# Kernel optimization log

Hardware: AMD Instinct MI355X
Metric: run time of the kernel (lower is better)

## Reference

```python
import jax, jax.numpy as jnp
import numpy as np

HIDDEN = 128
LR = 0.01          # epsilon (energy optimizer Adam lr)
B1, B2, EPS = 0.9, 0.999, 1e-8  # torch.optim.Adam defaults


def rho(s):
    return jnp.clip(s, 0.0, 1.0)


def setup_inputs() -> dict:
    key = jax.random.key(0)
    k_x, k_w0, k_w1 = jax.random.split(key, 3)
    input_size, output_size = 262144, 1024
    x = jax.random.uniform(k_x, (input_size,), dtype=jnp.float32)
    # xavier_uniform as in nn.init.xavier_uniform_
    lim0 = float(np.sqrt(6.0 / (input_size + HIDDEN)))
    W0 = jax.random.uniform(k_w0, (input_size, HIDDEN), jnp.float32, -lim0, lim0)
    lim1 = float(np.sqrt(6.0 / (HIDDEN + output_size)))
    W1 = jax.random.uniform(k_w1, (HIDDEN, output_size), jnp.float32, -lim1, lim1)
    b0 = jnp.zeros((input_size,), jnp.float32)
    b1 = jnp.zeros((HIDDEN,), jnp.float32)
    b2 = jnp.zeros((output_size,), jnp.float32)
    return {"x": x, "b0": b0, "b1": b1, "b2": b2, "W0": W0, "W1": W1,
            "n_iterations": 20}


def reference(x, b0, b1, b2, W0, W1, n_iterations):
    # Energy: sum ||rho(layer)||^2/2 - sum rho(layer).b - sum rho(pre) W rho(post)
    def energy(h, o):
        rx, rh, ro = rho(x), rho(h), rho(o)
        sq = 0.5 * (rx @ rx + rh @ rh + ro @ ro)
        lin = -(rx @ b0 + rh @ b1 + ro @ b2)
        quad = -((rx @ W0) @ rh + (rh @ W1) @ ro)
        return sq + lin + quad

    grad_e = jax.grad(energy, argnums=(0, 1))

    def adam_update(s, m, v, g, t):
        m = B1 * m + (1.0 - B1) * g
        v = B2 * v + (1.0 - B2) * (g * g)
        m_hat = m / (1.0 - jnp.power(jnp.float32(B1), t))
        v_hat = v / (1.0 - jnp.power(jnp.float32(B2), t))
        s = s - LR * m_hat / (jnp.sqrt(v_hat) + EPS)
        return s, m, v

    def step(carry, _):
        h, o, mh, vh, mo, vo, t = carry
        t = t + 1.0
        gh, go = grad_e(h, o)
        h, mh, vh = adam_update(h, mh, vh, gh, t)
        o, mo, vo = adam_update(o, mo, vo, go, t)
        return (h, o, mh, vh, mo, vo, t), None

    z_h = jnp.zeros_like(b1)  # hidden state starts at zeros
    z_o = jnp.zeros_like(b2)  # output state starts at zeros
    carry0 = (z_h, z_o, z_h, z_h, z_o, z_o, jnp.float32(0.0))
    (h, o, *_), _ = jax.lax.scan(step, carry0, None, length=int(n_iterations))
    return o
```

## Files before the change

kernel.cpp:

```cpp
#include <hip/hip_runtime.h>
#include <math.h>

#define NBLK_B 8

__device__ __forceinline__ float rho(float s) {
  return fminf(fmaxf(s, 0.0f), 1.0f);
}

__device__ __forceinline__ float drho(float s) {
  if (s < 0.0f || s > 1.0f) return 0.0f;
  float g = 1.0f;
  if (s == 0.0f) g *= 0.5f;
  if (s == 1.0f) g *= 0.5f;
  return g;
}

template <int ROWS>
__global__ __launch_bounds__(256) void k1_xw0(const float* __restrict__ x,
                                              const float* __restrict__ W0,
                                              float* __restrict__ part,
                                              int* __restrict__ flags) {
  __shared__ float xs[ROWS];
  __shared__ float red[8][132];
  const int t = threadIdx.x;
  const int b = blockIdx.x;
  if (b == 0 && t < NBLK_B) flags[t * 32] = 0;
  const int r0 = b * ROWS;
  for (int i = t; i < ROWS; i += 256) xs[i] = rho(x[r0 + i]);
  __syncthreads();
  const int cq = t & 31;
  const int rg = t >> 5;
  constexpr int GR = ROWS / 8;
  const float4* __restrict__ W4 = reinterpret_cast<const float4*>(W0);
  float ax = 0.f, ay = 0.f, az = 0.f, aw = 0.f;
  const int base = (r0 + rg * GR) * 32 + cq;
#pragma unroll 8
  for (int i = 0; i < GR; ++i) {
    const float xv = xs[rg * GR + i];
    const float4 w = W4[base + i * 32];
    ax = fmaf(xv, w.x, ax);
    ay = fmaf(xv, w.y, ay);
    az = fmaf(xv, w.z, az);
    aw = fmaf(xv, w.w, aw);
  }
  red[rg][cq * 4 + 0] = ax;
  red[rg][cq * 4 + 1] = ay;
  red[rg][cq * 4 + 2] = az;
  red[rg][cq * 4 + 3] = aw;
  __syncthreads();
  if (t < 128) {
    float s = 0.f;
#pragma unroll
    for (int g = 0; g < 8; ++g) s += red[g][t];
    part[b * 128 + t] = s;
  }
}

__global__ __launch_bounds__(256) void k2_iter(const float* __restrict__ part,
                                               const int npart,
                                               const float* __restrict__ W1,
                                               const float* __restrict__ b1,
                                               const float* __restrict__ b2,
                                               const int* __restrict__ niterp,
                                               float* __restrict__ c0part,
                                               float* __restrict__ aPartG,
                                               int* __restrict__ flags,
                                               float* __restrict__ out) {
  __shared__ float w1s[128 * 128];
  __shared__ float rhs_[128];
  __shared__ float ros_[128];
  __shared__ float c0s[128];
  __shared__ float b1s[128];
  __shared__ float bpart[2][128];
  __shared__ float apl[2][128];

  const int t = threadIdx.x;
  const int p = blockIdx.x;
  const int jk = t & 127;
  const int half = t >> 7;

  const float4* __restrict__ W14 = reinterpret_cast<const float4*>(W1);
#pragma unroll
  for (int itr = 0; itr < 16; ++itr) {
    const int e4 = itr * 256 + t;
    const int j = e4 >> 5;
    const int c4 = e4 & 31;
    const float4 w = W14[j * 256 + p * 32 + c4];
    const int rb = j * 128;
    const int sw = j & 31;
    const int c = c4 * 4;
    w1s[rb + ((c + 0) ^ sw)] = w.x;
    w1s[rb + ((c + 1) ^ sw)] = w.y;
    w1s[rb + ((c + 2) ^ sw)] = w.z;
    w1s[rb + ((c + 3) ^ sw)] = w.w;
  }
  {
    const int seg = npart >> 3;
    const int hseg = seg >> 1;
    float s = 0.f;
    const int rbase = p * seg + half * hseg;
#pragma unroll 8
    for (int q = 0; q < hseg; ++q) s += part[(rbase + q) * 128 + jk];
    bpart[half][jk] = s;
  }
  __syncthreads();
  if (half == 0)
    __hip_atomic_store(&c0part[p * 128 + jk], bpart[0][jk] + bpart[1][jk],
                       __ATOMIC_RELAXED, __HIP_MEMORY_SCOPE_AGENT);
  __syncthreads();
  if (t == 0) {
    __threadfence();
    __hip_atomic_store(&flags[p * 32], 1, __ATOMIC_RELEASE,
                       __HIP_MEMORY_SCOPE_AGENT);
  }
  if (half == 0) b1s[jk] = b1[jk];
  const float b2v = (half == 0) ? b2[p * 128 + jk] : 0.f;
  const int niter = *niterp;
  if (half == 0) { rhs_[jk] = 0.f; ros_[jk] = 0.f; }
  float hreg = 0.f, mh = 0.f, vh = 0.f;
  float oreg = 0.f, mo = 0.f, vo = 0.f;
  if (t < NBLK_B) {
    while (__hip_atomic_load(&flags[t * 32], __ATOMIC_ACQUIRE,
                             __HIP_MEMORY_SCOPE_AGENT) < 1)
      __builtin_amdgcn_s_sleep(1);
  }
  __syncthreads();
  if (half == 0) {
    float s = 0.f;
#pragma unroll
    for (int q = 0; q < NBLK_B; ++q)
      s += __hip_atomic_load(&c0part[q * 128 + jk], __ATOMIC_RELAXED,
                             __HIP_MEMORY_SCOPE_AGENT);
    c0s[jk] = s;
  }
  __syncthreads();

  for (int it = 1; it <= niter; ++it) {
    const int par = it & 1;
    const int x0 = half * 64;
    float accA = 0.f;
#pragma unroll 8
    for (int u = 0; u < 64; ++u) {
      const int c = x0 + u;
      accA = fmaf(w1s[jk * 128 + (c ^ (jk & 31))], ros_[c], accA);
    }
    apl[half][jk] = accA;
    __syncthreads();
    if (half == 0)
      __hip_atomic_store(&aPartG[par * 1024 + p * 128 + jk],
                         apl[0][jk] + apl[1][jk], __ATOMIC_RELAXED,
                         __HIP_MEMORY_SCOPE_AGENT);
    __syncthreads();
    if (t == 0) {
      __threadfence();
      __hip_atomic_store(&flags[p * 32], it + 1, __ATOMIC_RELEASE,
                         __HIP_MEMORY_SCOPE_AGENT);
    }
    float accB = 0.f;
#pragma unroll 8
    for (int u = 0; u < 64; ++u) {
      const int j = x0 + u;
      accB = fmaf(rhs_[j], w1s[j * 128 + (jk ^ (j & 31))], accB);
    }
    bpart[half][jk] = accB;
    __syncthreads();
    if (t < NBLK_B) {
      while (__hip_atomic_load(&flags[t * 32], __ATOMIC_ACQUIRE,
                               __HIP_MEMORY_SCOPE_AGENT) < it + 1)
        __builtin_amdgcn_s_sleep(1);
    }
    __syncthreads();
    if (half == 0) {
      const float bsum = bpart[0][jk] + bpart[1][jk];
      float a = 0.f;
#pragma unroll
      for (int q = 0; q < NBLK_B; ++q)
        a += __hip_atomic_load(&aPartG[par * 1024 + q * 128 + jk],
                               __ATOMIC_RELAXED, __HIP_MEMORY_SCOPE_AGENT);
      const float tf = (float)it;
      const float bc1 = 1.0f - powf(0.9f, tf);
      const float bc2 = 1.0f - powf(0.999f, tf);
      {
        const float gh = drho(hreg) * (rhs_[jk] - b1s[jk] - c0s[jk] - a);
        mh = 0.9f * mh + 0.1f * gh;
        vh = 0.999f * vh + 0.001f * (gh * gh);
        hreg = hreg - 0.01f * (mh / bc1) / (sqrtf(vh / bc2) + 1e-8f);
      }
      {
        const float go = drho(oreg) * (ros_[jk] - b2v - bsum);
        mo = 0.9f * mo + 0.1f * go;
        vo = 0.999f * vo + 0.001f * (go * go);
        oreg = oreg - 0.01f * (mo / bc1) / (sqrtf(vo / bc2) + 1e-8f);
      }
      rhs_[jk] = rho(hreg);
      ros_[jk] = rho(oreg);
    }
    __syncthreads();
  }
  if (half == 0) out[p * 128 + jk] = oreg;
}

extern "C" void kernel_launch(void* const* d_in, const int* in_sizes, int n_in,
                              void* d_out, int out_size, void* d_ws,
                              size_t ws_size, hipStream_t stream) {
  const float* x  = (const float*)d_in[0];
  const float* b1 = (const float*)d_in[2];
  const float* b2 = (const float*)d_in[3];
  const float* W0 = (const float*)d_in[4];
  const float* W1 = (const float*)d_in[5];
  const int*   ni = (const int*)d_in[6];
  float* out = (float*)d_out;

  char* ws = (char*)d_ws;
  int*   flags  = (int*)ws;
  float* c0part = (float*)(ws + 1024);
  float* aPartG = (float*)(ws + 1024 + 4096);
  float* part   = (float*)(ws + 13312);

  const int nrows = in_sizes[0];
  const size_t hdr = 13312;
  int nblk;
  if (ws_size >= hdr + (size_t)(nrows / 256) * 512) {
    nblk = nrows / 256;
    hipLaunchKernelGGL(k1_xw0<256>, dim3(nblk), dim3(256), 0, stream,
                       x, W0, part, flags);
  } else if (ws_size >= hdr + (size_t)(nrows / 512) * 512) {
    nblk = nrows / 512;
    hipLaunchKernelGGL(k1_xw0<512>, dim3(nblk), dim3(256), 0, stream,
                       x, W0, part, flags);
  } else {
    nblk = nrows / 1024;
    hipLaunchKernelGGL(k1_xw0<1024>, dim3(nblk), dim3(256), 0, stream,
                       x, W0, part, flags);
  }
  hipLaunchKernelGGL(k2_iter, dim3(NBLK_B), dim3(256), 0, stream,
                     part, nblk, W1, b1, b2, ni, c0part, aPartG, flags, out);
}
```

Baseline: 100.6 us.

## Pipeline the hidden/output updates with a one-iteration lag on cross-block flags

The iteration loop is reordered so each block first updates its output slice from purely local data. It then computes the W1·rho(o) partial for the next iteration and publishes it. The hidden update consumes the partial published one iteration earlier, so blocks only wait for flag value `it`, using a 4-slot ring buffer, which hides the inter-block synchronisation latency. The initial bias reduction is also done redundantly by every block, dropping the c0part exchange and one global wait, and the inner dot products now use four accumulators for ILP. The cost is redundant reads of the partial-sum buffer and subtler correctness reasoning about slot reuse.

```diff
diff --git a/kernel.cpp b/kernel.cpp
--- a/kernel.cpp
+++ b/kernel.cpp
@@ -62,7 +62,6 @@
                                                const float* __restrict__ b1,
                                                const float* __restrict__ b2,
                                                const int* __restrict__ niterp,
-                                               float* __restrict__ c0part,
                                                float* __restrict__ aPartG,
                                                int* __restrict__ flags,
                                                float* __restrict__ out) {
@@ -73,6 +72,7 @@
   __shared__ float b1s[128];
   __shared__ float bpart[2][128];
   __shared__ float apl[2][128];
+  __shared__ float red[8][132];
 
   const int t = threadIdx.x;
   const int p = blockIdx.x;
@@ -95,59 +95,87 @@
     w1s[rb + ((c + 3) ^ sw)] = w.w;
   }
   {
-    const int seg = npart >> 3;
-    const int hseg = seg >> 1;
+    const int cq = t & 31;
+    const int rg = t >> 5;
+    const float4* __restrict__ p4 = reinterpret_cast<const float4*>(part);
+    float ax = 0.f, ay = 0.f, az = 0.f, aw = 0.f;
+    for (int r = rg; r < npart; r += 8) {
+      const float4 v = p4[r * 32 + cq];
+      ax += v.x; ay += v.y; az += v.z; aw += v.w;
+    }
+    red[rg][cq * 4 + 0] = ax;
+    red[rg][cq * 4 + 1] = ay;
+    red[rg][cq * 4 + 2] = az;
+    red[rg][cq * 4 + 3] = aw;
+  }
+  const int niter = *niterp;
+  const float b2v = (half == 0) ? b2[p * 128 + jk] : 0.f;
+  __syncthreads();
+  if (half == 0) {
     float s = 0.f;
-    const int rbase = p * seg + half * hseg;
-#pragma unroll 8
-    for (int q = 0; q < hseg; ++q) s += part[(rbase + q) * 128 + jk];
-    bpart[half][jk] = s;
-  }
-  __syncthreads();
-  if (half == 0)
-    __hip_atomic_store(&c0part[p * 128 + jk], bpart[0][jk] + bpart[1][jk],
+#pragma unroll
+    for (int g = 0; g < 8; ++g) s += red[g][jk];
+    c0s[jk] = s;
+    b1s[jk] = b1[jk];
+    rhs_[jk] = 0.f;
+    ros_[jk] = 0.f;
+    __hip_atomic_store(&aPartG[1 * 1024 + p * 128 + jk], 0.f,
                        __ATOMIC_RELAXED, __HIP_MEMORY_SCOPE_AGENT);
+  }
   __syncthreads();
   if (t == 0) {
     __threadfence();
     __hip_atomic_store(&flags[p * 32], 1, __ATOMIC_RELEASE,
                        __HIP_MEMORY_SCOPE_AGENT);
   }
-  if (half == 0) b1s[jk] = b1[jk];
-  const float b2v = (half == 0) ? b2[p * 128 + jk] : 0.f;
-  const int niter = *niterp;
-  if (half == 0) { rhs_[jk] = 0.f; ros_[jk] = 0.f; }
+
   float hreg = 0.f, mh = 0.f, vh = 0.f;
   float oreg = 0.f, mo = 0.f, vo = 0.f;
-  if (t < NBLK_B) {
-    while (__hip_atomic_load(&flags[t * 32], __ATOMIC_ACQUIRE,
-                             __HIP_MEMORY_SCOPE_AGENT) < 1)
-      __builtin_amdgcn_s_sleep(1);
-  }
-  __syncthreads();
-  if (half == 0) {
-    float s = 0.f;
-#pragma unroll
-    for (int q = 0; q < NBLK_B; ++q)
-      s += __hip_atomic_load(&c0part[q * 128 + jk], __ATOMIC_RELAXED,
-                             __HIP_MEMORY_SCOPE_AGENT);
-    c0s[jk] = s;
-  }
-  __syncthreads();
+  const int x0 = half * 64;
 
   for (int it = 1; it <= niter; ++it) {
-    const int par = it & 1;
-    const int x0 = half * 64;
-    float accA = 0.f;
-#pragma unroll 8
-    for (int u = 0; u < 64; ++u) {
-      const int c = x0 + u;
-      accA = fmaf(w1s[jk * 128 + (c ^ (jk & 31))], ros_[c], accA);
-    }
-    apl[half][jk] = accA;
-    __syncthreads();
+    const float tf = (float)it;
+    const float bc1 = 1.0f - powf(0.9f, tf);
+    const float bc2 = 1.0f - powf(0.999f, tf);
+    {
+      float a0 = 0.f, a1 = 0.f, a2 = 0.f, a3 = 0.f;
+#pragma unroll 4
+      for (int u = 0; u < 64; u += 4) {
+        const int j0 = x0 + u;
+        a0 = fmaf(rhs_[j0 + 0], w1s[(j0 + 0) * 128 + (jk ^ ((j0 + 0) & 31))], a0);
+        a1 = fmaf(rhs_[j0 + 1], w1s[(j0 + 1) * 128 + (jk ^ ((j0 + 1) & 31))], a1);
+        a2 = fmaf(rhs_[j0 + 2], w1s[(j0 + 2) * 128 + (jk ^ ((j0 + 2) & 31))], a2);
+        a3 = fmaf(rhs_[j0 + 3], w1s[(j0 + 3) * 128 + (jk ^ ((j0 + 3) & 31))], a3);
+      }
+      bpart[half][jk] = (a0 + a1) + (a2 + a3);
+    }
+    __syncthreads();
+    if (half == 0) {
+      const float bsum = bpart[0][jk] + bpart[1][jk];
+      const float rot = rho(oreg);
+      const float go = drho(oreg) * (rot - b2v - bsum);
+      mo = 0.9f * mo + 0.1f * go;
+      vo = 0.999f * vo + 0.001f * (go * go);
+      oreg = oreg - 0.01f * (mo / bc1) / (sqrtf(vo / bc2) + 1e-8f);
+      ros_[jk] = rho(oreg);
+    }
+    __syncthreads();
+    {
+      float a0 = 0.f, a1 = 0.f, a2 = 0.f, a3 = 0.f;
+#pragma unroll 4
+      for (int u = 0; u < 64; u += 4) {
+        const int c0i = x0 + u;
+        a0 = fmaf(w1s[jk * 128 + ((c0i + 0) ^ (jk & 31))], ros_[c0i + 0], a0);
+        a1 = fmaf(w1s[jk * 128 + ((c0i + 1) ^ (jk & 31))], ros_[c0i + 1], a1);
+        a2 = fmaf(w1s[jk * 128 + ((c0i + 2) ^ (jk & 31))], ros_[c0i + 2], a2);
+        a3 = fmaf(w1s[jk * 128 + ((c0i + 3) ^ (jk & 31))], ros_[c0i + 3], a3);
+      }
+      apl[half][jk] = (a0 + a1) + (a2 + a3);
+    }
+    __syncthreads();
+    const int wslot = (it + 1) & 3;
     if (half == 0)
-      __hip_atomic_store(&aPartG[par * 1024 + p * 128 + jk],
+      __hip_atomic_store(&aPartG[wslot * 1024 + p * 128 + jk],
                          apl[0][jk] + apl[1][jk], __ATOMIC_RELAXED,
                          __HIP_MEMORY_SCOPE_AGENT);
     __syncthreads();
@@ -156,44 +184,24 @@
       __hip_atomic_store(&flags[p * 32], it + 1, __ATOMIC_RELEASE,
                          __HIP_MEMORY_SCOPE_AGENT);
     }
-    float accB = 0.f;
-#pragma unroll 8
-    for (int u = 0; u < 64; ++u) {
-      const int j = x0 + u;
-      accB = fmaf(rhs_[j], w1s[j * 128 + (jk ^ (j & 31))], accB);
-    }
-    bpart[half][jk] = accB;
-    __syncthreads();
     if (t < NBLK_B) {
       while (__hip_atomic_load(&flags[t * 32], __ATOMIC_ACQUIRE,
-                               __HIP_MEMORY_SCOPE_AGENT) < it + 1)
+                               __HIP_MEMORY_SCOPE_AGENT) < it)
         __builtin_amdgcn_s_sleep(1);
     }
     __syncthreads();
     if (half == 0) {
-      const float bsum = bpart[0][jk] + bpart[1][jk];
+      const int rslot = it & 3;
       float a = 0.f;
 #pragma unroll
       for (int q = 0; q < NBLK_B; ++q)
-        a += __hip_atomic_load(&aPartG[par * 1024 + q * 128 + jk],
+        a += __hip_atomic_load(&aPartG[rslot * 1024 + q * 128 + jk],
                                __ATOMIC_RELAXED, __HIP_MEMORY_SCOPE_AGENT);
-      const float tf = (float)it;
-      const float bc1 = 1.0f - powf(0.9f, tf);
-      const float bc2 = 1.0f - powf(0.999f, tf);
-      {
-        const float gh = drho(hreg) * (rhs_[jk] - b1s[jk] - c0s[jk] - a);
-        mh = 0.9f * mh + 0.1f * gh;
-        vh = 0.999f * vh + 0.001f * (gh * gh);
-        hreg = hreg - 0.01f * (mh / bc1) / (sqrtf(vh / bc2) + 1e-8f);
-      }
-      {
-        const float go = drho(oreg) * (ros_[jk] - b2v - bsum);
-        mo = 0.9f * mo + 0.1f * go;
-        vo = 0.999f * vo + 0.001f * (go * go);
-        oreg = oreg - 0.01f * (mo / bc1) / (sqrtf(vo / bc2) + 1e-8f);
-      }
+      const float gh = drho(hreg) * (rhs_[jk] - b1s[jk] - c0s[jk] - a);
+      mh = 0.9f * mh + 0.1f * gh;
+      vh = 0.999f * vh + 0.001f * (gh * gh);
+      hreg = hreg - 0.01f * (mh / bc1) / (sqrtf(vh / bc2) + 1e-8f);
       rhs_[jk] = rho(hreg);
-      ros_[jk] = rho(oreg);
     }
     __syncthreads();
   }
@@ -213,12 +221,11 @@
 
   char* ws = (char*)d_ws;
   int*   flags  = (int*)ws;
-  float* c0part = (float*)(ws + 1024);
-  float* aPartG = (float*)(ws + 1024 + 4096);
-  float* part   = (float*)(ws + 13312);
+  float* aPartG = (float*)(ws + 1024);
+  float* part   = (float*)(ws + 1024 + 16384);
 
   const int nrows = in_sizes[0];
-  const size_t hdr = 13312;
+  const size_t hdr = 1024 + 16384;
   int nblk;
   if (ws_size >= hdr + (size_t)(nrows / 256) * 512) {
     nblk = nrows / 256;
@@ -234,5 +241,5 @@
                        x, W0, part, flags);
   }
   hipLaunchKernelGGL(k2_iter, dim3(NBLK_B), dim3(256), 0, stream,
-                     part, nblk, W1, b1, b2, ni, c0part, aPartG, flags, out);
-}
+                     part, nblk, W1, b1, b2, ni, aPartG, flags, out);
+}
```

New measurement: 145.9 us. 45.0% more time.
